# Kernel optimization log

Hardware: AMD Instinct MI355X
Metric: run time of the kernel (lower is better)

The kernel has to match this reference:

```python
import jax, jax.numpy as jnp
import numpy as np

EXPAND = 1

def setup_inputs() -> dict:
    key = jax.random.key(0)
    k1, k2 = jax.random.split(key)
    B = 2097152
    pre = jax.random.normal(k1, (B, 25), dtype=jnp.float32)
    tar = jax.random.normal(k2, (B, 25), dtype=jnp.float32)
    return {"pre": pre, "tar": tar}

def reference(pre, tar):
    B = pre.shape[0]
    # 6 independent 4-way softmaxes per sample, scaled by 3*expand
    logits = pre[:, :24].reshape(B, 6, 4)
    out = (3.0 * EXPAND) * jax.nn.softmax(logits, axis=-1)  # [B, 6, 4]
    # out[24] = relu(pre[:,24]) in the original, but loss only uses out[0:24],
    # so the relu does not affect the returned loss.
    diff = out.reshape(B, 24) - tar[:, :24]
    # per-sample mean over 24 elems, then mean over batch
    per_sample = jnp.mean(diff * diff, axis=-1)  # [B]
    return jnp.mean(per_sample)
```

## Files before the change

kernel.cpp:

```cpp
#include <hip/hip_runtime.h>


constexpr int B_ROWS   = 2097152;
constexpr int ROWW     = 25;
constexpr int TILE_ROWS = 256;
constexpr int NTHREADS = 256;
constexpr int NBLOCKS  = 2048;
constexpr int NTILES   = B_ROWS / TILE_ROWS;
constexpr int TILE_F4  = TILE_ROWS * ROWW / 4;

__global__ __launch_bounds__(NTHREADS)
void soft_add_partial(const float* __restrict__ pre,
                      const float* __restrict__ tar,
                      float* __restrict__ partial)
{
    __shared__ float s_pre[TILE_ROWS * ROWW];
    __shared__ float s_tar[TILE_ROWS * ROWW];
    __shared__ float s_red[NTHREADS / 64];

    const int tid = threadIdx.x;
    float acc = 0.0f;

    for (int tile = blockIdx.x; tile < NTILES; tile += gridDim.x) {
        const long base = (long)tile * TILE_ROWS * ROWW;
        const float4* gp = reinterpret_cast<const float4*>(pre + base);
        const float4* gt = reinterpret_cast<const float4*>(tar + base);
        float4* sp = reinterpret_cast<float4*>(s_pre);
        float4* st = reinterpret_cast<float4*>(s_tar);

        for (int i = tid; i < TILE_F4; i += NTHREADS) {
            sp[i] = gp[i];
            st[i] = gt[i];
        }
        __syncthreads();

        const float* rp = s_pre + tid * ROWW;
        const float* rt = s_tar + tid * ROWW;
        #pragma unroll
        for (int g = 0; g < 6; ++g) {
            const float v0 = rp[4*g + 0];
            const float v1 = rp[4*g + 1];
            const float v2 = rp[4*g + 2];
            const float v3 = rp[4*g + 3];
            const float m  = fmaxf(fmaxf(v0, v1), fmaxf(v2, v3));
            const float e0 = __expf(v0 - m);
            const float e1 = __expf(v1 - m);
            const float e2 = __expf(v2 - m);
            const float e3 = __expf(v3 - m);
            const float r  = 3.0f / (e0 + e1 + e2 + e3);
            const float d0 = e0 * r - rt[4*g + 0];
            const float d1 = e1 * r - rt[4*g + 1];
            const float d2 = e2 * r - rt[4*g + 2];
            const float d3 = e3 * r - rt[4*g + 3];
            acc += d0 * d0;
            acc += d1 * d1;
            acc += d2 * d2;
            acc += d3 * d3;
        }
        __syncthreads();
    }

    #pragma unroll
    for (int off = 32; off > 0; off >>= 1)
        acc += __shfl_down(acc, off, 64);
    const int wave = tid >> 6;
    const int lane = tid & 63;
    if (lane == 0) s_red[wave] = acc;
    __syncthreads();
    if (tid == 0) {
        float s = 0.0f;
        #pragma unroll
        for (int w = 0; w < NTHREADS / 64; ++w) s += s_red[w];
        partial[blockIdx.x] = s;
    }
}

__global__ __launch_bounds__(NTHREADS)
void soft_add_final(const float* __restrict__ partial, float* __restrict__ out)
{
    __shared__ float s_red[NTHREADS / 64];
    const int tid = threadIdx.x;
    float acc = 0.0f;
    for (int i = tid; i < NBLOCKS; i += NTHREADS)
        acc += partial[i];
    #pragma unroll
    for (int off = 32; off > 0; off >>= 1)
        acc += __shfl_down(acc, off, 64);
    const int wave = tid >> 6;
    const int lane = tid & 63;
    if (lane == 0) s_red[wave] = acc;
    __syncthreads();
    if (tid == 0) {
        float s = 0.0f;
        #pragma unroll
        for (int w = 0; w < NTHREADS / 64; ++w) s += s_red[w];
        out[0] = s * (1.0f / (24.0f * (float)B_ROWS));
    }
}

extern "C" void kernel_launch(void* const* d_in, const int* in_sizes, int n_in,
                              void* d_out, int out_size, void* d_ws, size_t ws_size,
                              hipStream_t stream)
{
    const float* pre = (const float*)d_in[0];
    const float* tar = (const float*)d_in[1];
    float* out = (float*)d_out;
    float* partial = (float*)d_ws;

    soft_add_partial<<<NBLOCKS, NTHREADS, 0, stream>>>(pre, tar, partial);
    soft_add_final<<<1, NTHREADS, 0, stream>>>(partial, out);
}
```

Baseline: 84.40 us.

## Use single-wave blocks, keep targets in registers, fuse final reduction via atomic counter

Replaces the 256-thread, two-buffer tiled kernel with 64-thread single-wave blocks that each process a contiguous run of 64-row tiles. Targets are loaded coalesced into registers and never staged in shared memory. Softmax outputs are written back into the shared pre tile and compared in the coalesced layout. The separate final-reduction kernel is replaced by a last-block-done pattern using an atomic counter, at the cost of an extra memset launch and three barriers per tile.

```diff
diff --git a/kernel.cpp b/kernel.cpp
--- a/kernel.cpp
+++ b/kernel.cpp
@@ -3,59 +3,87 @@
 
 constexpr int B_ROWS   = 2097152;
 constexpr int ROWW     = 25;
-constexpr int TILE_ROWS = 256;
-constexpr int NTHREADS = 256;
-constexpr int NBLOCKS  = 2048;
-constexpr int NTILES   = B_ROWS / TILE_ROWS;
-constexpr int TILE_F4  = TILE_ROWS * ROWW / 4;
+constexpr int WTILE    = 64;
+constexpr int NTHREADS = 64;
+constexpr int NBLOCKS  = 4096;
+constexpr int NTILES   = B_ROWS / WTILE;
+constexpr int TPB      = NTILES / NBLOCKS;
+constexpr int TILE_F4  = WTILE * ROWW / 4;
 
 __global__ __launch_bounds__(NTHREADS)
-void soft_add_partial(const float* __restrict__ pre,
-                      const float* __restrict__ tar,
-                      float* __restrict__ partial)
+void soft_add_fused(const float* __restrict__ pre,
+                    const float* __restrict__ tar,
+                    float* __restrict__ out,
+                    float* __restrict__ partial,
+                    unsigned int* __restrict__ counter)
 {
-    __shared__ float s_pre[TILE_ROWS * ROWW];
-    __shared__ float s_tar[TILE_ROWS * ROWW];
-    __shared__ float s_red[NTHREADS / 64];
+    __shared__ float s_pre[WTILE * ROWW];
+    const int lane = threadIdx.x;
+    const int bid  = blockIdx.x;
 
-    const int tid = threadIdx.x;
     float acc = 0.0f;
 
-    for (int tile = blockIdx.x; tile < NTILES; tile += gridDim.x) {
-        const long base = (long)tile * TILE_ROWS * ROWW;
+    for (int k = 0; k < TPB; ++k) {
+        const long t = (long)bid * TPB + k;
+        const long base = t * (WTILE * ROWW);
         const float4* gp = reinterpret_cast<const float4*>(pre + base);
         const float4* gt = reinterpret_cast<const float4*>(tar + base);
         float4* sp = reinterpret_cast<float4*>(s_pre);
-        float4* st = reinterpret_cast<float4*>(s_tar);
 
-        for (int i = tid; i < TILE_F4; i += NTHREADS) {
-            sp[i] = gp[i];
-            st[i] = gt[i];
+        float4 rt[7], rp[7];
+        #pragma unroll
+        for (int j = 0; j < 7; ++j) {
+            const int i = lane + j * 64;
+            if (j < 6 || lane < 16) rt[j] = gt[i];
+        }
+        #pragma unroll
+        for (int j = 0; j < 7; ++j) {
+            const int i = lane + j * 64;
+            if (j < 6 || lane < 16) rp[j] = gp[i];
+        }
+        #pragma unroll
+        for (int j = 0; j < 7; ++j) {
+            const int i = lane + j * 64;
+            if (j < 6 || lane < 16) sp[i] = rp[j];
         }
         __syncthreads();
 
-        const float* rp = s_pre + tid * ROWW;
-        const float* rt = s_tar + tid * ROWW;
+        float* rowp = s_pre + lane * ROWW;
+        float o[24];
         #pragma unroll
         for (int g = 0; g < 6; ++g) {
-            const float v0 = rp[4*g + 0];
-            const float v1 = rp[4*g + 1];
-            const float v2 = rp[4*g + 2];
-            const float v3 = rp[4*g + 3];
+            const float v0 = rowp[4*g + 0];
+            const float v1 = rowp[4*g + 1];
+            const float v2 = rowp[4*g + 2];
+            const float v3 = rowp[4*g + 3];
             const float m  = fmaxf(fmaxf(v0, v1), fmaxf(v2, v3));
             const float e0 = __expf(v0 - m);
             const float e1 = __expf(v1 - m);
             const float e2 = __expf(v2 - m);
             const float e3 = __expf(v3 - m);
             const float r  = 3.0f / (e0 + e1 + e2 + e3);
-            const float d0 = e0 * r - rt[4*g + 0];
-            const float d1 = e1 * r - rt[4*g + 1];
-            const float d2 = e2 * r - rt[4*g + 2];
-            const float d3 = e3 * r - rt[4*g + 3];
-            acc += d0 * d0;
-            acc += d1 * d1;
-            acc += d2 * d2;
-            acc += d3 * d3;
+            o[4*g + 0] = e0 * r;
+            o[4*g + 1] = e1 * r;
+            o[4*g + 2] = e2 * r;
+            o[4*g + 3] = e3 * r;
+        }
+        #pragma unroll
+        for (int m2 = 0; m2 < 24; ++m2) rowp[m2] = o[m2];
+        __syncthreads();
+
+        #pragma unroll
+        for (int j = 0; j < 7; ++j) {
+            const int i = lane + j * 64;
+            if (j < 6 || lane < 16) {
+                const float4 ov = sp[i];
+                const float4 tv = rt[j];
+                int col = (4 * i) % 25;
+                float d;
+                d = ov.x - tv.x; if (col != 24) acc += d * d; col = (col == 24) ? 0 : col + 1;
+                d = ov.y - tv.y; if (col != 24) acc += d * d; col = (col == 24) ? 0 : col + 1;
+                d = ov.z - tv.z; if (col != 24) acc += d * d; col = (col == 24) ? 0 : col + 1;
+                d = ov.w - tv.w; if (col != 24) acc += d * d;
+            }
         }
         __syncthreads();
     }
@@ -63,38 +91,24 @@
     #pragma unroll
     for (int off = 32; off > 0; off >>= 1)
         acc += __shfl_down(acc, off, 64);
-    const int wave = tid >> 6;
-    const int lane = tid & 63;
-    if (lane == 0) s_red[wave] = acc;
-    __syncthreads();
-    if (tid == 0) {
+
+    unsigned int prev = 0;
+    if (lane == 0) {
+        partial[bid] = acc;
+        __threadfence();
+        prev = atomicAdd(counter, 1u);
+    }
+    prev = __shfl(prev, 0, 64);
+    if (prev == NBLOCKS - 1) {
+        __threadfence();
         float s = 0.0f;
+        for (int i = lane; i < NBLOCKS; i += 64)
+            s += partial[i];
         #pragma unroll
-        for (int w = 0; w < NTHREADS / 64; ++w) s += s_red[w];
-        partial[blockIdx.x] = s;
-    }
-}
-
-__global__ __launch_bounds__(NTHREADS)
-void soft_add_final(const float* __restrict__ partial, float* __restrict__ out)
-{
-    __shared__ float s_red[NTHREADS / 64];
-    const int tid = threadIdx.x;
-    float acc = 0.0f;
-    for (int i = tid; i < NBLOCKS; i += NTHREADS)
-        acc += partial[i];
-    #pragma unroll
-    for (int off = 32; off > 0; off >>= 1)
-        acc += __shfl_down(acc, off, 64);
-    const int wave = tid >> 6;
-    const int lane = tid & 63;
-    if (lane == 0) s_red[wave] = acc;
-    __syncthreads();
-    if (tid == 0) {
-        float s = 0.0f;
-        #pragma unroll
-        for (int w = 0; w < NTHREADS / 64; ++w) s += s_red[w];
-        out[0] = s * (1.0f / (24.0f * (float)B_ROWS));
+        for (int off = 32; off > 0; off >>= 1)
+            s += __shfl_down(s, off, 64);
+        if (lane == 0)
+            out[0] = s * (1.0f / (24.0f * (float)B_ROWS));
     }
 }
 
@@ -106,7 +120,8 @@
     const float* tar = (const float*)d_in[1];
     float* out = (float*)d_out;
     float* partial = (float*)d_ws;
+    unsigned int* counter = (unsigned int*)((char*)d_ws + NBLOCKS * sizeof(float));
 
-    soft_add_partial<<<NBLOCKS, NTHREADS, 0, stream>>>(pre, tar, partial);
-    soft_add_final<<<1, NTHREADS, 0, stream>>>(partial, out);
+    hipMemsetAsync(counter, 0, sizeof(unsigned int), stream);
+    soft_add_fused<<<NBLOCKS, NTHREADS, 0, stream>>>(pre, tar, out, partial, counter);
 }
```

Result: slower. 323.1 us (+282.9%).
